# Performance work log

Measured on AMD Instinct MI355X. Metric: run time of the kernel, lower is better.

The kernel has to match this reference:

```python
import jax, jax.numpy as jnp
import numpy as np

B, S, D, H, L, FF, V = 2, 1024, 1024, 16, 4, 2048, 32000
DK = D // H
EPS = 1e-5  # torch LayerNorm default


def _pos_enc(n, d):
    # matches torch PositionalEncoding: pe[pos, 2i]=sin, pe[pos, 2i+1]=cos
    pos = jnp.arange(n, dtype=jnp.float32)[:, None]
    div = jnp.exp(jnp.arange(0, d, 2, dtype=jnp.float32) * (-jnp.log(10000.0) / d))
    pe = jnp.zeros((n, d), dtype=jnp.float32)
    pe = pe.at[:, 0::2].set(jnp.sin(pos * div))
    pe = pe.at[:, 1::2].set(jnp.cos(pos * div))
    return pe


def setup_inputs() -> dict:
    key = jax.random.key(0)
    ks = jax.random.split(key, 12)
    s = 0.02
    return {
        "tokens": jax.random.randint(ks[0], (B, S), 0, V, dtype=jnp.int32),
        "emb": jax.random.normal(ks[1], (V, D), jnp.float32) * s,
        "Wq": jax.random.normal(ks[2], (L, D, D), jnp.float32) * s,
        "bq": jnp.zeros((L, D), jnp.float32),
        "Wk": jax.random.normal(ks[3], (L, D, D), jnp.float32) * s,
        "bk": jnp.zeros((L, D), jnp.float32),
        "Wv": jax.random.normal(ks[4], (L, D, D), jnp.float32) * s,
        "bv": jnp.zeros((L, D), jnp.float32),
        "Wo": jax.random.normal(ks[5], (L, D, D), jnp.float32) * s,
        "bo": jnp.zeros((L, D), jnp.float32),
        "W1": jax.random.normal(ks[6], (L, D, FF), jnp.float32) * s,
        "b1": jnp.zeros((L, FF), jnp.float32),
        "W2": jax.random.normal(ks[7], (L, FF, D), jnp.float32) * s,
        "b2": jnp.zeros((L, D), jnp.float32),
        "gamma": jnp.ones((L, D), jnp.float32),
        "beta": jnp.zeros((L, D), jnp.float32),
    }


def _layernorm(x, g, b):
    mu = jnp.mean(x, axis=-1, keepdims=True)
    var = jnp.mean(jnp.square(x - mu), axis=-1, keepdims=True)
    return (x - mu) * jax.lax.rsqrt(var + EPS) * g + b


def _encoder_layer(x, p):
    Wq, bq, Wk, bk, Wv, bv, Wo, bo, W1, b1, W2, b2, g, be = p
    # naive MHA: explicit QK^T / softmax / AV, materializing [B,H,S,S]
    q = (x @ Wq + bq).reshape(B, S, H, DK).transpose(0, 2, 1, 3)
    k = (x @ Wk + bk).reshape(B, S, H, DK).transpose(0, 2, 1, 3)
    v = (x @ Wv + bv).reshape(B, S, H, DK).transpose(0, 2, 1, 3)
    scores = jnp.einsum("bhqd,bhkd->bhqk", q, k) / jnp.sqrt(jnp.float32(DK))
    attn = jax.nn.softmax(scores, axis=-1)
    o = jnp.einsum("bhqk,bhkd->bhqd", attn, v)
    o = o.transpose(0, 2, 1, 3).reshape(B, S, D) @ Wo + bo
    # NOTE: same LayerNorm params used twice, as in the original module
    x = _layernorm(x + o, g, be)
    f = jax.nn.relu(x @ W1 + b1) @ W2 + b2
    x = _layernorm(x + f, g, be)
    return x, None


def reference(tokens, emb, Wq, bq, Wk, bk, Wv, bv, Wo, bo, W1, b1, W2, b2, gamma, beta):
    x = emb[tokens]  # [B,S,D]
    # faithful to the original bug: pe[:x.size(0)] indexes the BATCH dim,
    # pe slice has shape [B,1,D] and broadcasts over the sequence dim
    x = x + _pos_enc(B, D)[:, None, :]
    params = (Wq, bq, Wk, bk, Wv, bv, Wo, bo, W1, b1, W2, b2, gamma, beta)
    x, _ = jax.lax.scan(_encoder_layer, x, params)
    return x
```

## Files before the change

kernel.cpp:

```cpp
#include <hip/hip_runtime.h>
#include <cstdint>
#include <cstddef>

#define Bx 2
#define Sx 1024
#define Dx 1024
#define Hx 16
#define Lx 4
#define FFx 2048
#define DKx 64
#define Mx (Bx * Sx)

typedef __attribute__((ext_vector_type(4))) float f32x4;
typedef __attribute__((ext_vector_type(8))) __bf16 bf16x8;
typedef __attribute__((ext_vector_type(4))) __bf16 bf16x4;
typedef __attribute__((ext_vector_type(2))) __bf16 bf16x2;

__global__ void embed_kernel(const int* __restrict__ tokens,
                             const float* __restrict__ emb,
                             float* __restrict__ x, __bf16* __restrict__ xb) {
  size_t i = (size_t)blockIdx.x * blockDim.x + threadIdx.x;
  if (i >= (size_t)Mx * Dx / 2) return;
  int p = (int)(i % (Dx / 2));
  size_t bs = i / (Dx / 2);
  int b = (int)(bs >> 10);
  int tok = tokens[bs];
  float arg = (float)b * expf((float)(2 * p) * (-logf(10000.0f) / (float)Dx));
  float sv, cv;
  __sincosf(arg, &sv, &cv);
  const float2 e = ((const float2*)(emb + (size_t)tok * Dx))[p];
  float2 o;
  o.x = e.x + sv;
  o.y = e.y + cv;
  ((float2*)x)[i] = o;
  bf16x2 ob;
  ob[0] = (__bf16)o.x;
  ob[1] = (__bf16)o.y;
  ((bf16x2*)xb)[i] = ob;
}

__global__ void transpose_to_bf16(const float* __restrict__ W, __bf16* __restrict__ Wt,
                                  int K, int N, size_t sstride, size_t dstride) {
  __shared__ float tile[32][33];
  const float* Ws = W + blockIdx.z * sstride;
  __bf16* Wd = Wt + blockIdx.z * dstride;
  int tx = threadIdx.x, ty = threadIdx.y;
  int n0 = blockIdx.x * 32, k0 = blockIdx.y * 32;
#pragma unroll
  for (int i = 0; i < 4; ++i)
    tile[ty + 8 * i][tx] = Ws[(size_t)(k0 + ty + 8 * i) * N + n0 + tx];
  __syncthreads();
#pragma unroll
  for (int i = 0; i < 4; ++i)
    Wd[(size_t)(n0 + ty + 8 * i) * K + k0 + tx] = (__bf16)tile[tx][ty + 8 * i];
}

struct T4Args {
  const float* s0; const float* s1; const float* s2; const float* s3;
  __bf16* d0; __bf16* d1; __bf16* d2; __bf16* d3;
};
__global__ void transpose4_to_bf16(T4Args a) {
  __shared__ float tile[32][33];
  const int zz = blockIdx.z, l = zz >> 2, which = zz & 3;
  const size_t M1c = (size_t)Dx * Dx;
  const float* Ws = (which == 0 ? a.s0 : which == 1 ? a.s1 : which == 2 ? a.s2 : a.s3) + (size_t)l * M1c;
  __bf16* Wd = (which == 0)   ? a.d0 + (size_t)l * 3 * M1c
               : (which == 1) ? a.d1 + (size_t)l * 3 * M1c
               : (which == 2) ? a.d2 + (size_t)l * 3 * M1c
                              : a.d3 + (size_t)l * M1c;
  int tx = threadIdx.x, ty = threadIdx.y;
  int n0 = blockIdx.x * 32, k0 = blockIdx.y * 32;
#pragma unroll
  for (int i = 0; i < 4; ++i)
    tile[ty + 8 * i][tx] = Ws[(size_t)(k0 + ty + 8 * i) * Dx + n0 + tx];
  __syncthreads();
#pragma unroll
  for (int i = 0; i < 4; ++i)
    Wd[(size_t)(n0 + ty + 8 * i) * Dx + k0 + tx] = (__bf16)tile[tx][ty + 8 * i];
}

__global__ void concat3_kernel(const float* __restrict__ a, const float* __restrict__ b,
                               const float* __restrict__ c, float* __restrict__ out) {
  int i = blockIdx.x * 256 + threadIdx.x;
  int l = i / 3072, j = i % 3072;
  float v = (j < 1024) ? a[l * 1024 + j]
                       : ((j < 2048) ? b[l * 1024 + j - 1024] : c[l * 1024 + j - 2048]);
  out[i] = v;
}

__device__ __forceinline__ void xcd_swz_xy(int& bx, int& by) {
  const int nwg = gridDim.x * gridDim.y;
  int flat = by * gridDim.x + bx;
  flat = (flat & 7) * (nwg >> 3) + (flat >> 3);
  bx = flat % gridDim.x;
  by = flat / gridDim.x;
}

__device__ __forceinline__ void gld_lds16(const void* g, void* l) {
  __builtin_amdgcn_global_load_lds(
      (const __attribute__((address_space(1))) void*)(uintptr_t)g,
      (__attribute__((address_space(3))) void*)(uintptr_t)l, 16, 0, 0);
}

template <int TM, int TN, bool RELU, typename OutT, bool VOUT = false>
__global__ __launch_bounds__(256) void gemm_bt(const __bf16* __restrict__ A,
                                               const __bf16* __restrict__ Bt,
                                               const float* __restrict__ bias,
                                               OutT* __restrict__ C0,
                                               float* __restrict__ C1,
                                               __bf16* __restrict__ VT,
                                               int Kstep, int Kld, int ldc) {
  static_assert((TM + TN) == 192, "NCH fixed at 12");
  static_assert(!VOUT || TN == 64, "VOUT path assumes TN=64/WC=0");
  __shared__ __align__(16) __bf16 lds[3][(TM + TN) * 32];
  const int t = threadIdx.x;
  const int w = t >> 6, lane = t & 63;
  const int quad = lane >> 4, l16 = lane & 15;
  int bx = blockIdx.x, by = blockIdx.y;
  xcd_swz_xy(bx, by);
  const int m0 = by * TM, n0 = bx * TN;
  const int lr = lane >> 2, lc = (lane & 3) * 8;
  const int koff = blockIdx.z * Kstep;

  f32x4 acc[2][4] = {};

  const int WR = (TN == 128) ? (w >> 1) * (TM / 2) : w * (TM / 4);
  const int WC = (TN == 128) ? (w & 1) * 64 : 0;
  const __bf16* Abase = A + (size_t)m0 * Kld + koff;
  const __bf16* Bbase = Bt + (size_t)n0 * Kld + koff;

  auto stage = [&](int buf, int k0) {
#pragma unroll
    for (int c = 0; c < 3; ++c) {
      const int ch = c * 4 + w;
      const int r = ch * 16 + lr;
      const __bf16* g = (r < TM) ? (Abase + (size_t)r * Kld + k0 + lc)
                                 : (Bbase + (size_t)(r - TM) * Kld + k0 + lc);
      gld_lds16(g, (void*)(&lds[buf][0] + ch * 512));
    }
  };

  stage(0, 0);
  stage(1, 32);

  int cur = 0;
  for (int k0 = 0; k0 < Kstep; k0 += 32) {
    if (k0 + 32 < Kstep)
      asm volatile("s_waitcnt vmcnt(3) lgkmcnt(0)" ::: "memory");
    else
      asm volatile("s_waitcnt vmcnt(0) lgkmcnt(0)" ::: "memory");
    __builtin_amdgcn_s_barrier();
    __builtin_amdgcn_sched_barrier(0);

    int wb = cur + 2;
    if (wb >= 3) wb -= 3;
    if (k0 + 64 < Kstep) stage(wb, k0 + 64);

    bf16x8 af[2], bfr[4];
#pragma unroll
    for (int i = 0; i < 2; ++i)
      af[i] = *(const bf16x8*)&lds[cur][(WR + i * 16 + l16) * 32 + quad * 8];
#pragma unroll
    for (int j = 0; j < 4; ++j)
      bfr[j] = *(const bf16x8*)&lds[cur][(TM + WC + j * 16 + l16) * 32 + quad * 8];
    __builtin_amdgcn_s_setprio(1);
#pragma unroll
    for (int i = 0; i < 2; ++i)
#pragma unroll
      for (int j = 0; j < 4; ++j)
        acc[i][j] = __builtin_amdgcn_mfma_f32_16x16x32_bf16(af[i], bfr[j], acc[i][j], 0, 0, 0);
    __builtin_amdgcn_s_setprio(0);
    cur = (cur + 1 == 3) ? 0 : cur + 1;
  }

  const int col0 = n0 + WC + l16;

  if (VOUT && n0 >= 2048) {
    __syncthreads();
    __bf16* ldsf = &lds[0][0];
#pragma unroll
    for (int j = 0; j < 4; ++j) {
      const float bn = bias[col0 + j * 16];
      const int nl = (l16 + j * 16) * 136;
#pragma unroll
      for (int i = 0; i < 2; ++i)
#pragma unroll
        for (int r = 0; r < 4; ++r)
          ldsf[nl + WR + i * 16 + quad * 4 + r] = (__bf16)(acc[i][j][r] + bn);
    }
    __syncthreads();
    const int b = m0 >> 10;
    const int sbase = m0 & 1023;
    const int row = t >> 2, seg = t & 3;
    __bf16* vrow = VT + (size_t)(b * 1024 + (n0 - 2048) + row) * Sx + sbase + seg * 32;
    const __bf16* lrow = ldsf + row * 136 + seg * 32;
#pragma unroll
    for (int q = 0; q < 4; ++q)
      *(bf16x8*)(vrow + q * 8) = *(const bf16x8*)(lrow + q * 8);
    return;
  }

  const bool z0 = (blockIdx.z == 0);
#pragma unroll
  for (int j = 0; j < 4; ++j) {
    const int n = col0 + j * 16;
    const float bn = z0 ? bias[n] : 0.f;
#pragma unroll
    for (int i = 0; i < 2; ++i) {
#pragma unroll
      for (int r = 0; r < 4; ++r) {
        const int m = m0 + WR + i * 16 + quad * 4 + r;
        float v = acc[i][j][r] + bn;
        if (RELU) v = fmaxf(v, 0.f);
        if (z0)
          C0[(size_t)m * ldc + n] = (OutT)v;
        else
          C1[(size_t)m * ldc + n] = v;
      }
    }
  }
}

__global__ __launch_bounds__(256) void attention_mfma(const __bf16* __restrict__ QKV,
                                                      const __bf16* __restrict__ Vt,
                                                      __bf16* __restrict__ O) {
  __shared__ __align__(16) __bf16 Ks[2][64 * 72];
  __shared__ __align__(16) __bf16 Vs[2][64 * 72];
  __shared__ __align__(16) __bf16 Pl[64 * 72];

  const int t = threadIdx.x;
  const int w = t >> 6, lane = t & 63;
  const int quad = lane >> 4, l16 = lane & 15;
  int bx = blockIdx.x, by = blockIdx.y;
  xcd_swz_xy(bx, by);
  const int q0 = bx * 64;
  const int h = by, b = blockIdx.z;
  const size_t rowbase = (size_t)b * Sx;
  const int hoff = h * 64;

  const __bf16* qrow = QKV + (rowbase + q0 + w * 16 + l16) * 3072 + hoff;
  bf16x8 qf0 = *(const bf16x8*)(qrow + quad * 8);
  bf16x8 qf1 = *(const bf16x8*)(qrow + 32 + quad * 8);

  const __bf16* Kbase = QKV + rowbase * 3072 + 1024 + hoff;
  const __bf16* Vbase = Vt + (size_t)(b * Hx + h) * 64 * Sx;

  const int srow = t >> 2, sseg = t & 3;
  bf16x8 kp0, kp1, vp0, vp1;

  f32x4 oacc[4] = {};
  float lsum = 0.f;
  const float cs = 0.125f * 1.44269504089f;

  {
    const __bf16* kr = Kbase + (size_t)srow * 3072 + sseg * 16;
    kp0 = *(const bf16x8*)kr;
    kp1 = *(const bf16x8*)(kr + 8);
    const __bf16* vr = Vbase + (size_t)srow * Sx + sseg * 16;
    vp0 = *(const bf16x8*)vr;
    vp1 = *(const bf16x8*)(vr + 8);
    *(bf16x8*)&Ks[0][srow * 72 + sseg * 16] = kp0;
    *(bf16x8*)&Ks[0][srow * 72 + sseg * 16 + 8] = kp1;
    *(bf16x8*)&Vs[0][srow * 72 + sseg * 16] = vp0;
    *(bf16x8*)&Vs[0][srow * 72 + sseg * 16 + 8] = vp1;
  }
  __syncthreads();

  for (int kt = 0; kt < Sx / 64; ++kt) {
    const int cur = kt & 1;
    if (kt < Sx / 64 - 1) {
      const int kn = (kt + 1) * 64;
      const __bf16* kr = Kbase + (size_t)(kn + srow) * 3072 + sseg * 16;
      kp0 = *(const bf16x8*)kr;
      kp1 = *(const bf16x8*)(kr + 8);
      const __bf16* vr = Vbase + (size_t)srow * Sx + kn + sseg * 16;
      vp0 = *(const bf16x8*)vr;
      vp1 = *(const bf16x8*)(vr + 8);
    }

    f32x4 s[4] = {};
#pragma unroll
    for (int j = 0; j < 4; ++j) {
      bf16x8 b0 = *(const bf16x8*)&Ks[cur][(j * 16 + l16) * 72 + quad * 8];
      bf16x8 b1 = *(const bf16x8*)&Ks[cur][(j * 16 + l16) * 72 + 32 + quad * 8];
      s[j] = __builtin_amdgcn_mfma_f32_16x16x32_bf16(b0, qf0, s[j], 0, 0, 0);
      s[j] = __builtin_amdgcn_mfma_f32_16x16x32_bf16(b1, qf1, s[j], 0, 0, 0);
    }

#pragma unroll
    for (int j = 0; j < 4; ++j) {
#pragma unroll
      for (int r = 0; r < 4; ++r) s[j][r] = __builtin_exp2f(s[j][r] * cs);
      lsum += s[j][0] + s[j][1] + s[j][2] + s[j][3];
    }

    const int prow = (w * 16 + l16) * 72;
#pragma unroll
    for (int j = 0; j < 4; ++j) {
      bf16x4 pk;
#pragma unroll
      for (int r = 0; r < 4; ++r) pk[r] = (__bf16)s[j][r];
      *(bf16x4*)&Pl[prow + j * 16 + quad * 4] = pk;
    }
    bf16x8 pa0 = *(const bf16x8*)&Pl[prow + quad * 8];
    bf16x8 pa1 = *(const bf16x8*)&Pl[prow + 32 + quad * 8];

#pragma unroll
    for (int j = 0; j < 4; ++j) {
      bf16x8 vb0 = *(const bf16x8*)&Vs[cur][(j * 16 + l16) * 72 + quad * 8];
      bf16x8 vb1 = *(const bf16x8*)&Vs[cur][(j * 16 + l16) * 72 + 32 + quad * 8];
      oacc[j] = __builtin_amdgcn_mfma_f32_16x16x32_bf16(pa0, vb0, oacc[j], 0, 0, 0);
      oacc[j] = __builtin_amdgcn_mfma_f32_16x16x32_bf16(pa1, vb1, oacc[j], 0, 0, 0);
    }

    if (kt < Sx / 64 - 1) {
      const int nxt = 1 - cur;
      *(bf16x8*)&Ks[nxt][srow * 72 + sseg * 16] = kp0;
      *(bf16x8*)&Ks[nxt][srow * 72 + sseg * 16 + 8] = kp1;
      *(bf16x8*)&Vs[nxt][srow * 72 + sseg * 16] = vp0;
      *(bf16x8*)&Vs[nxt][srow * 72 + sseg * 16 + 8] = vp1;
    }
    __syncthreads();
  }

  lsum += __shfl_xor(lsum, 16);
  lsum += __shfl_xor(lsum, 32);
  const float inv = 1.f / lsum;
#pragma unroll
  for (int r = 0; r < 4; ++r) {
    const float invr = __shfl(inv, quad * 4 + r);
    const size_t orow = (rowbase + q0 + w * 16 + quad * 4 + r) * 1024 + hoff;
#pragma unroll
    for (int j = 0; j < 4; ++j) O[orow + j * 16 + l16] = (__bf16)(oacc[j][r] * invr);
  }
}

__global__ void add_ln_kernel(const float* __restrict__ x, const float* __restrict__ r0,
                              const float* __restrict__ r1,
                              const float* __restrict__ gamma, const float* __restrict__ beta,
                              float* __restrict__ out, __bf16* __restrict__ outb) {
  const int row = blockIdx.x, t = threadIdx.x;
  const int lane = t & 63, w = t >> 6;
  __shared__ float red[2][4];
  const f32x4* xr = (const f32x4*)(x + (size_t)row * Dx);
  const f32x4* a0 = (const f32x4*)(r0 + (size_t)row * Dx);
  const f32x4* a1 = (const f32x4*)(r1 + (size_t)row * Dx);
  f32x4 v = xr[t] + a0[t] + a1[t];
  float s = v[0] + v[1] + v[2] + v[3];
#pragma unroll
  for (int off = 1; off < 64; off <<= 1) s += __shfl_xor(s, off);
  if (lane == 0) red[0][w] = s;
  __syncthreads();
  const float mu = (red[0][0] + red[0][1] + red[0][2] + red[0][3]) * (1.f / Dx);
  f32x4 d = v - mu;
  float vs = d[0] * d[0] + d[1] * d[1] + d[2] * d[2] + d[3] * d[3];
#pragma unroll
  for (int off = 1; off < 64; off <<= 1) vs += __shfl_xor(vs, off);
  if (lane == 0) red[1][w] = vs;
  __syncthreads();
  const float is = rsqrtf((red[1][0] + red[1][1] + red[1][2] + red[1][3]) * (1.f / Dx) + 1e-5f);
  f32x4 g = ((const f32x4*)gamma)[t];
  f32x4 be = ((const f32x4*)beta)[t];
  f32x4 y = d * is * g + be;
  ((f32x4*)(out + (size_t)row * Dx))[t] = y;
  bf16x4 yb;
#pragma unroll
  for (int r = 0; r < 4; ++r) yb[r] = (__bf16)y[r];
  ((bf16x4*)(outb + (size_t)row * Dx))[t] = yb;
}

extern "C" void kernel_launch(void* const* d_in, const int* in_sizes, int n_in,
                              void* d_out, int out_size, void* d_ws, size_t ws_size,
                              hipStream_t stream) {
  const int* tokens = (const int*)d_in[0];
  const float* emb = (const float*)d_in[1];
  const float* Wq = (const float*)d_in[2];
  const float* bq = (const float*)d_in[3];
  const float* Wk = (const float*)d_in[4];
  const float* bk = (const float*)d_in[5];
  const float* Wv = (const float*)d_in[6];
  const float* bv = (const float*)d_in[7];
  const float* Wo = (const float*)d_in[8];
  const float* bo = (const float*)d_in[9];
  const float* W1 = (const float*)d_in[10];
  const float* b1 = (const float*)d_in[11];
  const float* W2 = (const float*)d_in[12];
  const float* b2 = (const float*)d_in[13];
  const float* gamma = (const float*)d_in[14];
  const float* beta = (const float*)d_in[15];

  const size_t M1 = 1024 * 1024;
  float* ws = (float*)d_ws;
  float* x = ws;
  float* tmp = ws + 2 * M1;
  __bf16* bfr = (__bf16*)(ws + 4 * M1);
  __bf16* xb = bfr;
  __bf16* qkvb = bfr + 2 * M1;
  __bf16* ob = bfr + 8 * M1;
  __bf16* h1b = bfr + 10 * M1;
  __bf16* Vt = bfr + 14 * M1;
  __bf16* WqkvT = bfr + 16 * M1;
  __bf16* WoT = bfr + 28 * M1;
  __bf16* W1T = bfr + 32 * M1;
  __bf16* W2T = bfr + 40 * M1;
  float* bqkv = (float*)(bfr + 48 * M1);
  float* tmp1 = (float*)qkvb;

  embed_kernel<<<((size_t)Mx * Dx / 2 + 255) / 256, 256, 0, stream>>>(tokens, emb, x, xb);

  dim3 tb(32, 8);
  T4Args t4{Wq, Wk, Wv, Wo, WqkvT, WqkvT + M1, WqkvT + 2 * M1, WoT};
  transpose4_to_bf16<<<dim3(32, 32, 4 * Lx), tb, 0, stream>>>(t4);
  transpose_to_bf16<<<dim3(64, 32, Lx), tb, 0, stream>>>(W1, W1T, Dx, FFx, 2 * M1, 2 * M1);
  transpose_to_bf16<<<dim3(32, 64, Lx), tb, 0, stream>>>(W2, W2T, FFx, Dx, 2 * M1, 2 * M1);
  concat3_kernel<<<Lx * 12, 256, 0, stream>>>(bq, bk, bv, bqkv);

  for (int l = 0; l < Lx; ++l) {
    const __bf16* WqkvT_l = WqkvT + (size_t)l * 3 * M1;
    const __bf16* WoT_l = WoT + (size_t)l * M1;
    const __bf16* W1T_l = W1T + (size_t)l * 2 * M1;
    const __bf16* W2T_l = W2T + (size_t)l * 2 * M1;
    const float* bqkv_l = bqkv + (size_t)l * 3072;
    const float* bo_l = bo + (size_t)l * Dx;
    const float* b1_l = b1 + (size_t)l * FFx;
    const float* b2_l = b2 + (size_t)l * Dx;
    const float* g_l = gamma + (size_t)l * Dx;
    const float* be_l = beta + (size_t)l * Dx;

    gemm_bt<128, 64, false, __bf16, true><<<dim3(3072 / 64, Mx / 128, 1), 256, 0, stream>>>(
        xb, WqkvT_l, bqkv_l, qkvb, nullptr, Vt, Dx, Dx, 3072);

    attention_mfma<<<dim3(Sx / 64, Hx, Bx), 256, 0, stream>>>(qkvb, Vt, ob);

    gemm_bt<64, 128, false, float><<<dim3(Dx / 128, Mx / 64, 2), 256, 0, stream>>>(
        ob, WoT_l, bo_l, tmp, tmp1, nullptr, Dx / 2, Dx, Dx);
    add_ln_kernel<<<Mx, 256, 0, stream>>>(x, tmp, tmp1, g_l, be_l, x, xb);

    gemm_bt<128, 64, true, __bf16><<<dim3(FFx / 64, Mx / 128, 1), 256, 0, stream>>>(
        xb, W1T_l, b1_l, h1b, nullptr, nullptr, Dx, Dx, FFx);
    gemm_bt<64, 128, false, float><<<dim3(Dx / 128, Mx / 64, 2), 256, 0, stream>>>(
        h1b, W2T_l, b2_l, tmp, tmp1, nullptr, FFx / 2, FFx, Dx);
    add_ln_kernel<<<Mx, 256, 0, stream>>>(x, tmp, tmp1, g_l, be_l,
                                          (l == Lx - 1) ? (float*)d_out : x, xb);
  }
}
```

Before: 731.2 us.

## Stage attention K/V tiles via direct global-to-LDS loads with XOR swizzle

Replaces the register-staged K/V prefetch in the attention kernel with direct global-to-LDS loads (gld_lds16) into unpadded, XOR-swizzled shared tiles. The goal is to remove the register round trip and the ds_write instructions, and to shrink LDS use so more blocks fit per CU, with launch bounds raised to 3 blocks. It also raises wave priority around the MFMA groups and replaces __syncthreads with an explicit waitcnt plus barrier. The risk is that the swizzle mapping or the wait placement is wrong, and that attention is only part of the total model time.

```diff
diff --git a/kernel.cpp b/kernel.cpp
--- a/kernel.cpp
+++ b/kernel.cpp
@@ -221,11 +221,11 @@
   }
 }
 
-__global__ __launch_bounds__(256) void attention_mfma(const __bf16* __restrict__ QKV,
-                                                      const __bf16* __restrict__ Vt,
-                                                      __bf16* __restrict__ O) {
-  __shared__ __align__(16) __bf16 Ks[2][64 * 72];
-  __shared__ __align__(16) __bf16 Vs[2][64 * 72];
+__global__ __launch_bounds__(256, 3) void attention_mfma(const __bf16* __restrict__ QKV,
+                                                         const __bf16* __restrict__ Vt,
+                                                         __bf16* __restrict__ O) {
+  __shared__ __align__(16) __bf16 Ks[2][64 * 64];
+  __shared__ __align__(16) __bf16 Vs[2][64 * 64];
   __shared__ __align__(16) __bf16 Pl[64 * 72];
 
   const int t = threadIdx.x;
@@ -245,46 +245,41 @@
   const __bf16* Kbase = QKV + rowbase * 3072 + 1024 + hoff;
   const __bf16* Vbase = Vt + (size_t)(b * Hx + h) * 64 * Sx;
 
-  const int srow = t >> 2, sseg = t & 3;
-  bf16x8 kp0, kp1, vp0, vp1;
+  const int lrow = lane >> 3;
+  const int lcb = (lane & 7) ^ lrow;
+  auto stageKV = [&](int buf, int kt64) {
+#pragma unroll
+    for (int c = 0; c < 2; ++c) {
+      const int r8 = (c * 4 + w) * 8;
+      gld_lds16(Kbase + (size_t)(kt64 + r8 + lrow) * 3072 + lcb * 8,
+                (void*)&Ks[buf][(c * 4 + w) * 512]);
+      gld_lds16(Vbase + (size_t)(r8 + lrow) * 1024 + kt64 + lcb * 8,
+                (void*)&Vs[buf][(c * 4 + w) * 512]);
+    }
+  };
 
   f32x4 oacc[4] = {};
   float lsum = 0.f;
   const float cs = 0.125f * 1.44269504089f;
 
-  {
-    const __bf16* kr = Kbase + (size_t)srow * 3072 + sseg * 16;
-    kp0 = *(const bf16x8*)kr;
-    kp1 = *(const bf16x8*)(kr + 8);
-    const __bf16* vr = Vbase + (size_t)srow * Sx + sseg * 16;
-    vp0 = *(const bf16x8*)vr;
-    vp1 = *(const bf16x8*)(vr + 8);
-    *(bf16x8*)&Ks[0][srow * 72 + sseg * 16] = kp0;
-    *(bf16x8*)&Ks[0][srow * 72 + sseg * 16 + 8] = kp1;
-    *(bf16x8*)&Vs[0][srow * 72 + sseg * 16] = vp0;
-    *(bf16x8*)&Vs[0][srow * 72 + sseg * 16 + 8] = vp1;
-  }
-  __syncthreads();
-
+  stageKV(0, 0);
+  asm volatile("s_waitcnt vmcnt(0)" ::: "memory");
+  __builtin_amdgcn_s_barrier();
+
+  const int swz = l16 & 7;
   for (int kt = 0; kt < Sx / 64; ++kt) {
     const int cur = kt & 1;
-    if (kt < Sx / 64 - 1) {
-      const int kn = (kt + 1) * 64;
-      const __bf16* kr = Kbase + (size_t)(kn + srow) * 3072 + sseg * 16;
-      kp0 = *(const bf16x8*)kr;
-      kp1 = *(const bf16x8*)(kr + 8);
-      const __bf16* vr = Vbase + (size_t)srow * Sx + kn + sseg * 16;
-      vp0 = *(const bf16x8*)vr;
-      vp1 = *(const bf16x8*)(vr + 8);
-    }
+    if (kt < Sx / 64 - 1) stageKV(cur ^ 1, (kt + 1) * 64);
 
     f32x4 s[4] = {};
 #pragma unroll
     for (int j = 0; j < 4; ++j) {
-      bf16x8 b0 = *(const bf16x8*)&Ks[cur][(j * 16 + l16) * 72 + quad * 8];
-      bf16x8 b1 = *(const bf16x8*)&Ks[cur][(j * 16 + l16) * 72 + 32 + quad * 8];
+      bf16x8 b0 = *(const bf16x8*)&Ks[cur][(j * 16 + l16) * 64 + ((quad ^ swz) * 8)];
+      bf16x8 b1 = *(const bf16x8*)&Ks[cur][(j * 16 + l16) * 64 + (((4 + quad) ^ swz) * 8)];
+      __builtin_amdgcn_s_setprio(1);
       s[j] = __builtin_amdgcn_mfma_f32_16x16x32_bf16(b0, qf0, s[j], 0, 0, 0);
       s[j] = __builtin_amdgcn_mfma_f32_16x16x32_bf16(b1, qf1, s[j], 0, 0, 0);
+      __builtin_amdgcn_s_setprio(0);
     }
 
 #pragma unroll
@@ -307,20 +302,16 @@
 
 #pragma unroll
     for (int j = 0; j < 4; ++j) {
-      bf16x8 vb0 = *(const bf16x8*)&Vs[cur][(j * 16 + l16) * 72 + quad * 8];
-      bf16x8 vb1 = *(const bf16x8*)&Vs[cur][(j * 16 + l16) * 72 + 32 + quad * 8];
+      bf16x8 vb0 = *(const bf16x8*)&Vs[cur][(j * 16 + l16) * 64 + ((quad ^ swz) * 8)];
+      bf16x8 vb1 = *(const bf16x8*)&Vs[cur][(j * 16 + l16) * 64 + (((4 + quad) ^ swz) * 8)];
+      __builtin_amdgcn_s_setprio(1);
       oacc[j] = __builtin_amdgcn_mfma_f32_16x16x32_bf16(pa0, vb0, oacc[j], 0, 0, 0);
       oacc[j] = __builtin_amdgcn_mfma_f32_16x16x32_bf16(pa1, vb1, oacc[j], 0, 0, 0);
-    }
-
-    if (kt < Sx / 64 - 1) {
-      const int nxt = 1 - cur;
-      *(bf16x8*)&Ks[nxt][srow * 72 + sseg * 16] = kp0;
-      *(bf16x8*)&Ks[nxt][srow * 72 + sseg * 16 + 8] = kp1;
-      *(bf16x8*)&Vs[nxt][srow * 72 + sseg * 16] = vp0;
-      *(bf16x8*)&Vs[nxt][srow * 72 + sseg * 16 + 8] = vp1;
-    }
-    __syncthreads();
+      __builtin_amdgcn_s_setprio(0);
+    }
+
+    asm volatile("s_waitcnt vmcnt(0) lgkmcnt(0)" ::: "memory");
+    __builtin_amdgcn_s_barrier();
   }
 
   lsum += __shfl_xor(lsum, 16);
```

Result: no change. 727.1 us (-0.6%).
